# Optimization experiments

Measured on AMD Instinct MI355X. Metric: run time of the kernel, lower is better.

The kernel has to match this reference:

```python
import jax, jax.numpy as jnp
import numpy as np

ARCH = (1024, 2048, 2048, 512)
STEPS = 20
LR = 0.1
BATCH = 4096


def setup_inputs() -> dict:
    key = jax.random.key(0)
    ks = jax.random.split(key, 1 + len(ARCH) - 1)
    x = jax.random.normal(ks[0], (BATCH, ARCH[0]), dtype=jnp.float32)
    inp = {"x": x}
    # forward layers: weight (out, in) as in torch nn.Linear, orthogonal-ish init gain sqrt(2)
    for i in range(len(ARCH) - 1):
        fan_in = ARCH[i]
        W = jax.random.normal(ks[1 + i], (ARCH[i + 1], fan_in), dtype=jnp.float32) * jnp.sqrt(2.0 / fan_in)
        inp[f"W{i}"] = W
        inp[f"b{i}"] = jnp.zeros((ARCH[i + 1],), dtype=jnp.float32)
    return inp


def _errors(r, Ws):
    # errors[-1] = r[-1]; errors[i] = r[i] - tanh(F.linear(r[i+1], W_i.T)) = r[i] - tanh(r[i+1] @ W_i)
    errs = [None] * len(ARCH)
    errs[-1] = r[-1]
    for i in range(len(Ws) - 1, -1, -1):
        errs[i] = r[i] - jnp.tanh(r[i + 1] @ Ws[i])  # (B, arch[i])
    return errs


def _pc_forward(x, Ws, bs):
    # initialize states with a no-grad feedforward pass (torch.no_grad -> stop_gradient)
    r = [x]
    t = x
    for W, b in zip(Ws, bs):
        t = jnp.tanh(t @ W.T + b)
        r.append(jax.lax.stop_gradient(t))

    def step(carry, _):
        r = list(carry)
        errs = _errors(r, Ws)
        new_r = [r[0]]  # r[0] = x, fixed
        for i in range(1, len(ARCH)):
            feedback = errs[i - 1] @ Ws[i - 1].T  # F.linear(errors[i-1], W)
            new_r.append(r[i] + LR * (-errs[i] + feedback))
        return tuple(new_r), None

    r, _ = jax.lax.scan(step, tuple(r), None, length=STEPS)
    r = list(r)
    final_errs = _errors(r, Ws)
    total_error = 0.5 * sum(jnp.sum(e * e) for e in final_errs)
    return r[-1], total_error


def reference(x, W0, b0, W1, b1, W2, b2):
    Ws = [W0, W1, W2]
    bs = [b0, b1, b2]
    return _pc_forward(x, Ws, bs)
```

## Files before the change

kernel.cpp:

```cpp
#include <hip/hip_runtime.h>

typedef unsigned short u16;
typedef __bf16 bf16_t;
typedef bf16_t bf16x8 __attribute__((ext_vector_type(8)));
typedef u16 u16x8 __attribute__((ext_vector_type(8)));
typedef float f32x4 __attribute__((ext_vector_type(4)));

__device__ __forceinline__ u16 f2bf(float f) {
    unsigned u = __builtin_bit_cast(unsigned, f);
    u += 0x7fffu + ((u >> 16) & 1u);
    return (u16)(u >> 16);
}
__device__ __forceinline__ float bf2f(u16 h) {
    unsigned u = ((unsigned)h) << 16;
    return __builtin_bit_cast(float, u);
}
__device__ __forceinline__ float fast_tanh(float x) {
    x = fminf(fmaxf(x, -20.f), 20.f);
    float e = __expf(2.f * x);
    return (e - 1.f) * __builtin_amdgcn_rcpf(e + 1.f);
}
__device__ __forceinline__ void gload_lds16(const void* g, void* l) {
    __builtin_amdgcn_global_load_lds((__attribute__((address_space(1))) void*)(g),
                                     (__attribute__((address_space(3))) void*)(l),
                                     16, 0, 0);
}
__device__ __forceinline__ bf16x8 ld8(const u16* p) {
    return __builtin_bit_cast(bf16x8, *(const u16x8*)p);
}

#define VMW4() __builtin_amdgcn_s_waitcnt(0x3F74)
#define VMW0() __builtin_amdgcn_s_waitcnt(0x3F70)
#define MEMFENCE() asm volatile("" ::: "memory")

#define GATE() do { \
    MEMFENCE(); __builtin_amdgcn_s_barrier(); \
    asm volatile("s_waitcnt lgkmcnt(0)" ::: "memory"); \
    __builtin_amdgcn_sched_barrier(0); \
} while (0)
#define CLOSE() do { \
    __builtin_amdgcn_sched_barrier(0); \
    MEMFENCE(); __builtin_amdgcn_s_barrier(); MEMFENCE(); \
} while (0)



__global__ void cvt_bf16(const float* __restrict__ src, u16* __restrict__ dst, int n4) {
    int i = blockIdx.x * blockDim.x + threadIdx.x;
    if (i < n4) {
        float4 v = ((const float4*)src)[i];
        ushort4 o;
        o.x = f2bf(v.x); o.y = f2bf(v.y); o.z = f2bf(v.z); o.w = f2bf(v.w);
        ((ushort4*)dst)[i] = o;
    }
}

__global__ void transpose_cvt(const float* __restrict__ W, u16* __restrict__ WT, int R, int C) {
    __shared__ float tile[32][33];
    int c0 = blockIdx.x * 32, r0 = blockIdx.y * 32;
    int tx = threadIdx.x & 31, ty = threadIdx.x >> 5;
#pragma unroll
    for (int i = 0; i < 32; i += 8)
        tile[ty + i][tx] = W[(size_t)(r0 + ty + i) * C + (c0 + tx)];
    __syncthreads();
#pragma unroll
    for (int i = 0; i < 32; i += 8)
        WT[(size_t)(c0 + ty + i) * R + (r0 + tx)] = f2bf(tile[tx][ty + i]);
}

__global__ void blockify(const u16* __restrict__ src, u16* __restrict__ dst, int K) {
    const int nk = K >> 5;
    const int rb = blockIdx.x / nk, cb = blockIdx.x % nk;
    const int t = threadIdx.x;
    const int kloc = (t & 7) * 4;
    u16* d = dst + (size_t)blockIdx.x * 4096 + ((kloc >> 3) << 10) + (kloc & 7);
    const u16* s = src + (size_t)(rb * 128) * K + cb * 32 + kloc;
#pragma unroll
    for (int p = 0; p < 4; ++p) {
        int row = (t >> 3) + p * 32;
        *(ushort4*)(d + row * 8) = *(const ushort4*)(s + (size_t)row * K);
    }
}


struct Seg {
    const u16* A; const u16* B;
    const u16* rsrcb;
    const float* rsrcf;
    const float* bias;
    const u16* esub;
    float* outf;
    u16* outbf;
    int K, N, blkStart, mode, accum;
};
struct Phase {
    Seg seg[3];
    int bEnd0, bEnd1;
};

#define READ_A(buf, kk, mh) do { \
    const u16* _p = SH + (buf)*16384 + (wr2+(kk))*4096 + aoff + (mh)*512; \
    aR[0] = ld8(_p); aR[1] = ld8(_p+128); aR[2] = ld8(_p+256); aR[3] = ld8(_p+384); \
} while (0)

#define READ_B(buf, kk) do { \
    const u16* _p = SH + 32768 + (buf)*16384 + (wch2+(kk))*4096 + boff; \
    bR[0] = ld8(_p); bR[1] = ld8(_p+128); bR[2] = ld8(_p+256); bR[3] = ld8(_p+384); \
} while (0)

#define MFMA16(mh) do { \
    __builtin_amdgcn_s_setprio(1); \
    _Pragma("unroll") \
    for (int _i = 0; _i < 4; ++_i) { \
        _Pragma("unroll") \
        for (int _n = 0; _n < 4; ++_n) \
            acc[(mh)*4+_i][_n] = __builtin_amdgcn_mfma_f32_16x16x32_bf16( \
                aR[_i], bR[_n], acc[(mh)*4+_i][_n], 0, 0, 0); \
    } \
    __builtin_amdgcn_s_setprio(0); \
} while (0)

#define DO_PHASE(kk, mh, RB, STAGE_STMT, WAIT_STMT) do { \
    READ_A(buf, kk, mh); \
    if (RB) READ_B(buf, kk); \
    STAGE_STMT; \
    GATE(); \
    MFMA16(mh); \
    WAIT_STMT; \
    CLOSE(); \
} while (0)

__global__ __launch_bounds__(512, 2) void pc_phase(Phase ph, float* __restrict__ errAcc) {
    __shared__ __align__(16) u16 SH[65536];
    __shared__ float red[8];

    const int bid = blockIdx.x;
    const int segi = (bid >= ph.bEnd0 ? 1 : 0) + (bid >= ph.bEnd1 ? 1 : 0);

    const u16* Ab = ph.seg[segi].A;
    const u16* Bb = ph.seg[segi].B;
    const int K = ph.seg[segi].K;
    const int local = bid - ph.seg[segi].blkStart;
    const int bx2 = local >> 4;
    const int by2 = local & 15;
    const int nk32 = K >> 5, NT = K >> 6;

    const int tid  = threadIdx.x;
    const int wave = tid >> 6, lane = tid & 63;
    const int q    = lane >> 4, ln = lane & 15;
    const int wr = wave >> 2, wc = wave & 3;
    const int wr2 = wr * 2, wch2 = (wc >> 1) * 2;
    const int aoff = q * 1024 + ln * 8;
    const int boff = q * 1024 + ((wc & 1) * 64 + ln) * 8;

    const size_t t8 = (size_t)tid * 8;
    const u16* gA0 = Ab + ((size_t)(by2 * 2 + 0) * nk32) * 4096 + t8;
    const u16* gA1 = Ab + ((size_t)(by2 * 2 + 1) * nk32) * 4096 + t8;
    const u16* gB0 = Bb + ((size_t)(bx2 * 2 + 0) * nk32) * 4096 + t8;
    const u16* gB1 = Bb + ((size_t)(bx2 * 2 + 1) * nk32) * 4096 + t8;
    const int wb = wave * 512;

    auto stageA = [&](int cb, int bf, int ks) {
        const size_t g = (size_t)cb * 4096;
        u16* a = SH + bf * 16384 + ks * 4096 + wb;
        gload_lds16(gA0 + g, a);
        gload_lds16(gA1 + g, a + 8192);
    };
    auto stageB = [&](int cb, int bf, int ks) {
        const size_t g = (size_t)cb * 4096;
        u16* b = SH + 32768 + bf * 16384 + ks * 4096 + wb;
        gload_lds16(gB0 + g, b);
        gload_lds16(gB1 + g, b + 8192);
    };

    f32x4 acc[8][4];
#pragma unroll
    for (int i = 0; i < 8; ++i)
#pragma unroll
        for (int j = 0; j < 4; ++j)
            acc[i][j] = (f32x4){0.f, 0.f, 0.f, 0.f};

    stageA(0, 0, 0); stageB(0, 0, 0);
    stageA(1, 0, 1); stageB(1, 0, 1);
    VMW4();
    MEMFENCE(); __builtin_amdgcn_s_barrier(); MEMFENCE();

    bf16x8 aR[4], bR[4];

    for (int t = 0; t < NT - 1; ++t) {
        const int buf = t & 1, nbuf = buf ^ 1;
        const int cb0 = 2 * t + 2, cb1 = 2 * t + 3;
        DO_PHASE(0, 0, 1, stageA(cb0, nbuf, 0), (void)0);
        DO_PHASE(0, 1, 0, stageB(cb0, nbuf, 0), VMW4());
        DO_PHASE(1, 0, 1, stageA(cb1, nbuf, 1), (void)0);
        DO_PHASE(1, 1, 0, stageB(cb1, nbuf, 1), VMW4());
    }
    {
        const int buf = (NT - 1) & 1;
        DO_PHASE(0, 0, 1, (void)0, (void)0);
        DO_PHASE(0, 1, 0, (void)0, VMW0());
        DO_PHASE(1, 0, 1, (void)0, (void)0);
        DO_PHASE(1, 1, 0, (void)0, (void)0);
    }
    __syncthreads();

    const int N = ph.seg[segi].N;
    const int mode = ph.seg[segi].mode;
    const int accum = ph.seg[segi].accum;
    const u16* rsrcbP = ph.seg[segi].rsrcb;
    const float* rsrcfP = ph.seg[segi].rsrcf;
    const float* biasP = ph.seg[segi].bias;
    const u16* esubP = ph.seg[segi].esub;
    float* outfP = ph.seg[segi].outf;
    u16* outbfP = ph.seg[segi].outbf;

    const int nb32 = N >> 5;
    const size_t regOff = ((size_t)(by2 * 2 + wr) * nb32 + (size_t)(bx2 * 2 + (wc >> 1)) * 4) * 4096;
    u16* SLICE = SH + wave * 8192;

    float lsum = 0.f;
    const int rowg0 = by2 * 256 + wr * 128 + q * 4;
    const int colg0 = bx2 * 256 + wc * 64;

#pragma unroll
    for (int ct = 0; ct < 2; ++ct) {
        const size_t tileOff = regOff + (size_t)((wc & 1) * 2 + ct) * 4096;
        if (mode == 1 || mode == 2) {
#pragma unroll
            for (int p = 0; p < 8; ++p)
                *(u16x8*)(SLICE + p * 512 + lane * 8) =
                    *(const u16x8*)(rsrcbP + tileOff + p * 512 + lane * 8);
        }
        if (mode == 2) {
#pragma unroll
            for (int p = 0; p < 8; ++p)
                *(u16x8*)(SLICE + 4096 + p * 512 + lane * 8) =
                    *(const u16x8*)(esubP + tileOff + p * 512 + lane * 8);
        }
#pragma unroll
        for (int nh = 0; nh < 2; ++nh) {
            const int nt = ct * 2 + nh;
            const int ci = nh * 16 + ln;
            const int co = ((ci >> 3) & 3) * 1024 + (ci & 7);
            const int colg = colg0 + nt * 16 + ln;
            const float bnt = (mode == 0) ? biasP[colg] : 0.f;
#pragma unroll
            for (int mt = 0; mt < 8; ++mt) {
#pragma unroll
                for (int r = 0; r < 4; ++r) {
                    const int row = mt * 16 + q * 4 + r;
                    const int o = co + row * 8;
                    const float c = acc[mt][nt][r];
                    float v;
                    if (mode == 0) {
                        v = fast_tanh(c + bnt);
                        if (outfP) outfP[(size_t)(rowg0 + mt * 16 + r) * N + colg] = v;
                    } else if (mode == 1) {
                        v = bf2f(SLICE[o]) - fast_tanh(c);
                        if (accum) lsum += v * v;
                    } else if (mode == 2) {
                        v = bf2f(SLICE[o]) + 0.1f * (c - bf2f(SLICE[4096 + o]));
                    } else {
                        const size_t idx = (size_t)(rowg0 + mt * 16 + r) * N + colg;
                        v = 0.9f * rsrcfP[idx] + 0.1f * c;
                        outfP[idx] = v;
                        if (accum) lsum += v * v;
                    }
                    SLICE[o] = f2bf(v);
                }
            }
        }
#pragma unroll
        for (int p = 0; p < 8; ++p)
            *(u16x8*)(outbfP + tileOff + p * 512 + lane * 8) =
                *(const u16x8*)(SLICE + p * 512 + lane * 8);
    }

    if (accum) {
        lsum *= 0.5f;
#pragma unroll
        for (int o = 32; o > 0; o >>= 1) lsum += __shfl_down(lsum, o);
        if (lane == 0) red[wave] = lsum;
        __syncthreads();
        if (tid == 0) {
            float s = 0.f;
#pragma unroll
            for (int i = 0; i < 8; ++i) s += red[i];
            atomicAdd(errAcc, s);
        }
    }
}


extern "C" void kernel_launch(void* const* d_in, const int* in_sizes, int n_in,
                              void* d_out, int out_size, void* d_ws, size_t ws_size,
                              hipStream_t stream) {
    const float* x  = (const float*)d_in[0];
    const float* W0 = (const float*)d_in[1];
    const float* b0 = (const float*)d_in[2];
    const float* W1 = (const float*)d_in[3];
    const float* b1 = (const float*)d_in[4];
    const float* W2 = (const float*)d_in[5];
    const float* b2 = (const float*)d_in[6];

    const int Bz = 4096;

    char* ws = (char*)d_ws;
    size_t off = 0;
    auto alloc = [&](size_t bytes) -> char* {
        char* p = ws + off;
        off += (bytes + 255) & ~(size_t)255;
        return p;
    };

    u16*   r1b = (u16*)  alloc((size_t)Bz * 2048 * 2);
    u16*   r2b = (u16*)  alloc((size_t)Bz * 2048 * 2);
    u16*   r3b = (u16*)  alloc((size_t)Bz * 512 * 2);
    u16*   e0b = (u16*)  alloc((size_t)Bz * 1024 * 2);
    u16*   e1b = (u16*)  alloc((size_t)Bz * 2048 * 2);
    u16*   e2b = (u16*)  alloc((size_t)Bz * 2048 * 2);
    u16*   xb  = (u16*)  alloc((size_t)Bz * 1024 * 2);
    u16*   W0b = (u16*)  alloc((size_t)2048 * 1024 * 2);
    u16*   W0t = (u16*)  alloc((size_t)1024 * 2048 * 2);
    u16*   W1b = (u16*)  alloc((size_t)2048 * 2048 * 2);
    u16*   W1t = (u16*)  alloc((size_t)2048 * 2048 * 2);
    u16*   W2b = (u16*)  alloc((size_t)512 * 2048 * 2);
    u16*   W2t = (u16*)  alloc((size_t)2048 * 512 * 2);
    u16*   tmp = (u16*)  alloc((size_t)2048 * 2048 * 2);

    float* r3f    = (float*)d_out;
    float* errAcc = ((float*)d_out) + (size_t)Bz * 512;

    auto blkify = [&](const u16* s, u16* d, int M, int K) {
        blockify<<<(M / 128) * (K / 32), 256, 0, stream>>>(s, d, K);
    };

    cvt_bf16<<<(Bz * 1024 / 4) / 256, 256, 0, stream>>>(x, tmp, Bz * 1024 / 4);
    blkify(tmp, xb, Bz, 1024);
    cvt_bf16<<<(2048 * 1024 / 4) / 256, 256, 0, stream>>>(W0, tmp, 2048 * 1024 / 4);
    blkify(tmp, W0b, 2048, 1024);
    cvt_bf16<<<(2048 * 2048 / 4) / 256, 256, 0, stream>>>(W1, tmp, 2048 * 2048 / 4);
    blkify(tmp, W1b, 2048, 2048);
    cvt_bf16<<<(512 * 2048 / 4) / 256, 256, 0, stream>>>(W2, tmp, 512 * 2048 / 4);
    blkify(tmp, W2b, 512, 2048);
    transpose_cvt<<<dim3(1024 / 32, 2048 / 32), 256, 0, stream>>>(W0, tmp, 2048, 1024);
    blkify(tmp, W0t, 1024, 2048);
    transpose_cvt<<<dim3(2048 / 32, 2048 / 32), 256, 0, stream>>>(W1, tmp, 2048, 2048);
    blkify(tmp, W1t, 2048, 2048);
    transpose_cvt<<<dim3(2048 / 32, 512 / 32),  256, 0, stream>>>(W2, tmp, 512, 2048);
    blkify(tmp, W2t, 2048, 512);

    hipMemsetAsync(errAcc, 0, 4, stream);

    auto mkseg = [&](const u16* A, const u16* B, int K, int N,
                     const u16* rsrcb, const float* rsrcf, const float* bias,
                     const u16* esub, float* outf, u16* outbf,
                     int mode, int accum) {
        Seg s;
        s.A = A; s.B = B; s.rsrcb = rsrcb; s.rsrcf = rsrcf; s.bias = bias;
        s.esub = esub; s.outf = outf; s.outbf = outbf;
        s.K = K; s.N = N; s.blkStart = 0; s.mode = mode; s.accum = accum;
        return s;
    };
    auto nblk = [&](int N) { return (N / 256) * (Bz / 256); };

    auto launch1 = [&](Seg s0) {
        Phase ph;
        int b0c = nblk(s0.N);
        ph.seg[0] = s0; ph.seg[1] = s0; ph.seg[2] = s0;
        ph.bEnd0 = b0c; ph.bEnd1 = b0c;
        pc_phase<<<b0c, 512, 0, stream>>>(ph, errAcc);
    };
    auto launch3 = [&](Seg s0, Seg s1, Seg s2) {
        Phase ph;
        int b0c = nblk(s0.N), b1c = nblk(s1.N), b2c = nblk(s2.N);
        s1.blkStart = b0c; s2.blkStart = b0c + b1c;
        ph.seg[0] = s0; ph.seg[1] = s1; ph.seg[2] = s2;
        ph.bEnd0 = b0c; ph.bEnd1 = b0c + b1c;
        pc_phase<<<b0c + b1c + b2c, 512, 0, stream>>>(ph, errAcc);
    };

    launch1(mkseg(xb,  W0b, 1024, 2048, nullptr, nullptr, b0, nullptr, nullptr, r1b, 0, 0));
    launch1(mkseg(r1b, W1b, 2048, 2048, nullptr, nullptr, b1, nullptr, nullptr, r2b, 0, 0));
    launch1(mkseg(r2b, W2b, 2048, 512,  nullptr, nullptr, b2, nullptr, r3f,     r3b, 0, 0));

    for (int s = 0; s < 20; ++s) {
        int last = (s == 19) ? 1 : 0;
        launch3(mkseg(r2b, W1t, 2048, 2048, r1b, nullptr, nullptr, nullptr, nullptr, e1b, 1, 0),
                mkseg(r1b, W0t, 2048, 1024, xb,  nullptr, nullptr, nullptr, nullptr, e0b, 1, 0),
                mkseg(r3b, W2t, 512,  2048, r2b, nullptr, nullptr, nullptr, nullptr, e2b, 1, 0));
        launch3(mkseg(e1b, W1b, 2048, 2048, r2b, nullptr, nullptr, e2b, nullptr, r2b, 2, 0),
                mkseg(e2b, W2b, 2048, 512,  nullptr, r3f, nullptr, nullptr, r3f,  r3b, 3, last),
                mkseg(e0b, W0b, 1024, 2048, r1b, nullptr, nullptr, e1b, nullptr, r1b, 2, 0));
    }

    launch3(mkseg(r2b, W1t, 2048, 2048, r1b, nullptr, nullptr, nullptr, nullptr, e1b, 1, 1),
            mkseg(r1b, W0t, 2048, 1024, xb,  nullptr, nullptr, nullptr, nullptr, e0b, 1, 1),
            mkseg(r3b, W2t, 512,  2048, r2b, nullptr, nullptr, nullptr, nullptr, e2b, 1, 1));
}
```

Before: 3.605 ms.

## Replace per-phase barrier GEMM schedule with one barrier per tile and register ping-pong

The GEMM main loop used to run four gated phases per K-tile, each with two workgroup barriers and an lgkmcnt wait. It now uses a single vmcnt(0) wait and one barrier per tile. The A fragments are double-buffered in registers (aRe/aRo) so LDS reads for the next MFMA cluster are issued while the current one runs, and global-to-LDS staging of the next tile is interleaved with them. This is meant to cut barrier and stall overhead, at the cost of more VGPRs and a coarser wait on global loads.

```diff
diff --git a/kernel.cpp b/kernel.cpp
--- a/kernel.cpp
+++ b/kernel.cpp
@@ -29,19 +29,9 @@
     return __builtin_bit_cast(bf16x8, *(const u16x8*)p);
 }
 
-#define VMW4() __builtin_amdgcn_s_waitcnt(0x3F74)
 #define VMW0() __builtin_amdgcn_s_waitcnt(0x3F70)
 #define MEMFENCE() asm volatile("" ::: "memory")
-
-#define GATE() do { \
-    MEMFENCE(); __builtin_amdgcn_s_barrier(); \
-    asm volatile("s_waitcnt lgkmcnt(0)" ::: "memory"); \
-    __builtin_amdgcn_sched_barrier(0); \
-} while (0)
-#define CLOSE() do { \
-    __builtin_amdgcn_sched_barrier(0); \
-    MEMFENCE(); __builtin_amdgcn_s_barrier(); MEMFENCE(); \
-} while (0)
+#define SCHED0() __builtin_amdgcn_sched_barrier(0)
 
 
 
@@ -98,36 +88,26 @@
     int bEnd0, bEnd1;
 };
 
-#define READ_A(buf, kk, mh) do { \
-    const u16* _p = SH + (buf)*16384 + (wr2+(kk))*4096 + aoff + (mh)*512; \
-    aR[0] = ld8(_p); aR[1] = ld8(_p+128); aR[2] = ld8(_p+256); aR[3] = ld8(_p+384); \
+#define ISSUE_A(dst, kk, mh) do { \
+    const u16* _p = SH + buf * 16384 + (wr2 + (kk)) * 4096 + aoff + (mh) * 512; \
+    dst[0] = ld8(_p); dst[1] = ld8(_p + 128); dst[2] = ld8(_p + 256); dst[3] = ld8(_p + 384); \
 } while (0)
 
-#define READ_B(buf, kk) do { \
-    const u16* _p = SH + 32768 + (buf)*16384 + (wch2+(kk))*4096 + boff; \
-    bR[0] = ld8(_p); bR[1] = ld8(_p+128); bR[2] = ld8(_p+256); bR[3] = ld8(_p+384); \
+#define ISSUE_B(dst, kk) do { \
+    const u16* _p = SH + 32768 + buf * 16384 + (wch2 + (kk)) * 4096 + boff; \
+    dst[0] = ld8(_p); dst[1] = ld8(_p + 128); dst[2] = ld8(_p + 256); dst[3] = ld8(_p + 384); \
 } while (0)
 
-#define MFMA16(mh) do { \
+#define MFMACL(mh, A_, B_) do { \
     __builtin_amdgcn_s_setprio(1); \
     _Pragma("unroll") \
     for (int _i = 0; _i < 4; ++_i) { \
         _Pragma("unroll") \
         for (int _n = 0; _n < 4; ++_n) \
-            acc[(mh)*4+_i][_n] = __builtin_amdgcn_mfma_f32_16x16x32_bf16( \
-                aR[_i], bR[_n], acc[(mh)*4+_i][_n], 0, 0, 0); \
+            acc[(mh) * 4 + _i][_n] = __builtin_amdgcn_mfma_f32_16x16x32_bf16( \
+                A_[_i], B_[_n], acc[(mh) * 4 + _i][_n], 0, 0, 0); \
     } \
     __builtin_amdgcn_s_setprio(0); \
-} while (0)
-
-#define DO_PHASE(kk, mh, RB, STAGE_STMT, WAIT_STMT) do { \
-    READ_A(buf, kk, mh); \
-    if (RB) READ_B(buf, kk); \
-    STAGE_STMT; \
-    GATE(); \
-    MFMA16(mh); \
-    WAIT_STMT; \
-    CLOSE(); \
 } while (0)
 
 __global__ __launch_bounds__(512, 2) void pc_phase(Phase ph, float* __restrict__ errAcc) {
@@ -182,25 +162,25 @@
 
     stageA(0, 0, 0); stageB(0, 0, 0);
     stageA(1, 0, 1); stageB(1, 0, 1);
-    VMW4();
-    MEMFENCE(); __builtin_amdgcn_s_barrier(); MEMFENCE();
-
-    bf16x8 aR[4], bR[4];
-
-    for (int t = 0; t < NT - 1; ++t) {
+
+    bf16x8 aRe[4], aRo[4], bR[4];
+
+    for (int t = 0; t < NT; ++t) {
         const int buf = t & 1, nbuf = buf ^ 1;
-        const int cb0 = 2 * t + 2, cb1 = 2 * t + 3;
-        DO_PHASE(0, 0, 1, stageA(cb0, nbuf, 0), (void)0);
-        DO_PHASE(0, 1, 0, stageB(cb0, nbuf, 0), VMW4());
-        DO_PHASE(1, 0, 1, stageA(cb1, nbuf, 1), (void)0);
-        DO_PHASE(1, 1, 0, stageB(cb1, nbuf, 1), VMW4());
-    }
-    {
-        const int buf = (NT - 1) & 1;
-        DO_PHASE(0, 0, 1, (void)0, (void)0);
-        DO_PHASE(0, 1, 0, (void)0, VMW0());
-        DO_PHASE(1, 0, 1, (void)0, (void)0);
-        DO_PHASE(1, 1, 0, (void)0, (void)0);
+        const int more = (t + 1 < NT);
+        VMW0();
+        MEMFENCE(); __builtin_amdgcn_s_barrier(); MEMFENCE();
+
+        ISSUE_B(bR, 0); ISSUE_A(aRe, 0, 0); SCHED0();
+        if (more) { stageA(2 * t + 2, nbuf, 0); stageB(2 * t + 2, nbuf, 0); }
+        ISSUE_A(aRo, 0, 1); SCHED0();
+        MFMACL(0, aRe, bR); SCHED0();
+        if (more) { stageA(2 * t + 3, nbuf, 1); stageB(2 * t + 3, nbuf, 1); }
+        ISSUE_A(aRe, 1, 0); SCHED0();
+        MFMACL(1, aRo, bR); SCHED0();
+        ISSUE_B(bR, 1); ISSUE_A(aRo, 1, 1); SCHED0();
+        MFMACL(0, aRe, bR); SCHED0();
+        MFMACL(1, aRo, bR);
     }
     __syncthreads();
 
```

Result: slower. 4.053 ms (+12.4%).
